# Kernel optimization log

Measured on AMD Instinct MI355X. Metric: run time of the kernel, lower is better.

The kernel has to match this reference:

```python
import jax, jax.numpy as jnp
import numpy as np

GROUPS = 32
EPS = 1e-6


def group_norm(x, scale, bias):
    B, C, H, W = x.shape
    xg = x.reshape(B, GROUPS, C // GROUPS, H, W)
    mean = xg.mean(axis=(2, 3, 4), keepdims=True)
    var = xg.var(axis=(2, 3, 4), keepdims=True)
    xg = (xg - mean) * jax.lax.rsqrt(var + EPS)
    x = xg.reshape(B, C, H, W)
    return x * scale[None, :, None, None] + bias[None, :, None, None]


def conv1x1(x, w, b):
    # x: [B,C,H,W], w: [O,C], b: [O]
    return jnp.einsum('bchw,oc->bohw', x, w) + b[None, :, None, None]


def setup_inputs() -> dict:
    key = jax.random.key(0)
    ks = jax.random.split(key, 6)
    B, C, H, W = 8, 256, 64, 64
    s = 1.0 / np.sqrt(C)
    return {
        'x': jax.random.normal(ks[0], (B, C, H, W), dtype=jnp.float32),
        'gn_scale': jnp.ones((C,), dtype=jnp.float32),
        'gn_bias': jnp.zeros((C,), dtype=jnp.float32),
        'wq': jax.random.normal(ks[1], (C, C), dtype=jnp.float32) * s,
        'bq': jnp.zeros((C,), dtype=jnp.float32),
        'wk': jax.random.normal(ks[2], (C, C), dtype=jnp.float32) * s,
        'bk': jnp.zeros((C,), dtype=jnp.float32),
        'wv': jax.random.normal(ks[3], (C, C), dtype=jnp.float32) * s,
        'bv': jnp.zeros((C,), dtype=jnp.float32),
        'wo': jax.random.normal(ks[4], (C, C), dtype=jnp.float32) * s,
        'bo': jnp.zeros((C,), dtype=jnp.float32),
    }


def reference(x, gn_scale, gn_bias, wq, bq, wk, bk, wv, bv, wo, bo):
    skip = x
    h = group_norm(x, gn_scale, gn_bias)
    B, C, H, W = h.shape
    N = H * W
    q = conv1x1(h, wq, bq).reshape(B, C, N)  # [B,C,N]
    k = conv1x1(h, wk, bk).reshape(B, C, N)
    v = conv1x1(h, wv, bv).reshape(B, C, N)
    # scores[b,i,j] = sum_c q[b,c,i] k[b,c,j] / sqrt(C)
    scores = jnp.einsum('bci,bcj->bij', q, k) / jnp.sqrt(jnp.float32(C))
    a = jax.nn.softmax(scores, axis=2)  # softmax over keys j
    # z[b,c,i] = sum_j v[b,c,j] a[b,i,j]
    z = jnp.einsum('bcj,bij->bci', v, a).reshape(B, C, H, W)
    z = conv1x1(z, wo, bo)
    return skip + z
```

## Files before the change

kernel.cpp:

```cpp
#include <hip/hip_runtime.h>
#include <math.h>

typedef __bf16 bf16;
typedef __bf16 bf16x8 __attribute__((ext_vector_type(8)));
typedef __bf16 bf16x4 __attribute__((ext_vector_type(4)));
typedef float  f32x4  __attribute__((ext_vector_type(4)));
typedef float  f32x16 __attribute__((ext_vector_type(16)));
typedef unsigned int u32;
typedef unsigned char u8;
typedef u32 u32x2 __attribute__((ext_vector_type(2)));
typedef u32 u32x4 __attribute__((ext_vector_type(4)));
typedef int  i32x8 __attribute__((ext_vector_type(8)));

#define MFMA(a, b, c)   __builtin_amdgcn_mfma_f32_16x16x32_bf16((a), (b), (c), 0, 0, 0)
#define MFMAS(a, b, c)                                                           \
  __builtin_amdgcn_mfma_scale_f32_32x32x64_f8f6f4((a), (b), (c), 0, 0,           \
                                                  0, 0x7f7f7f7f, 0, 0x7f7f7f7f)

#define GLOAD_LDS16(g, l)                                                        \
  __builtin_amdgcn_global_load_lds(                                              \
      (const __attribute__((address_space(1))) void*)(g),                        \
      (__attribute__((address_space(3))) void*)(l), 16, 0, 0)

static constexpr int B_ = 8, C_ = 256, N_ = 4096;
static constexpr float QSCALE = 0.09016844005556021f;
static constexpr float PBIAS  = 2.0f;


static constexpr size_t HT_OFF = 0;
static constexpr size_t QT_OFF = 16777216;
static constexpr size_t KT_OFF = 25165824;
static constexpr size_t V_OFF  = 33554432;
static constexpr size_t WQ_OFF = 41943040;
static constexpr size_t WK_OFF = WQ_OFF + 131072;
static constexpr size_t WV_OFF = WK_OFF + 131072;
static constexpr size_t WO_OFF = WV_OFF + 131072;
static constexpr size_t LS_OFF = WO_OFF + 131072;
static constexpr size_t ZN2_OFF = LS_OFF + 524288;
static constexpr size_t PART_ELEMS = (size_t)B_ * C_ * N_;

__global__ __launch_bounds__(512) void gn_kernel(
    const float* __restrict__ x, const float* __restrict__ gsc, const float* __restrict__ gbi,
    bf16* __restrict__ hT,
    const float* __restrict__ wq, const float* __restrict__ wk,
    const float* __restrict__ wv, const float* __restrict__ wo,
    bf16* __restrict__ oq, bf16* __restrict__ ok, bf16* __restrict__ ov, bf16* __restrict__ oo) {
  int b = blockIdx.x >> 5, g = blockIdx.x & 31, c0 = g * 8;
  int t = threadIdx.x;
  if (t < 256) {
    int i = blockIdx.x * 256 + t;
    oq[i] = (bf16)wq[i];
    ok[i] = (bf16)wk[i];
    ov[i] = (bf16)wv[i];
    oo[i] = (bf16)wo[i];
  }
  const float* base = x + ((size_t)(b * C_ + c0)) * N_;
  __shared__ bf16 xl[32768];
  float s = 0.f, ss = 0.f;
  const f32x4* b4 = (const f32x4*)base;
#pragma unroll
  for (int p = 0; p < 16; p++) {
    int u = t + p * 512;
    f32x4 v = b4[u];
    s  += v[0] + v[1] + v[2] + v[3];
    ss += v[0] * v[0] + v[1] * v[1] + v[2] * v[2] + v[3] * v[3];
    bf16x4 xv;
#pragma unroll
    for (int e = 0; e < 4; e++) xv[e] = (bf16)v[e];
    *(bf16x4*)(xl + u * 4) = xv;
  }
#pragma unroll
  for (int off = 1; off < 64; off <<= 1) {
    s  += __shfl_xor(s, off);
    ss += __shfl_xor(ss, off);
  }
  __shared__ float red[16];
  if ((t & 63) == 0) { red[(t >> 6) * 2] = s; red[(t >> 6) * 2 + 1] = ss; }
  __syncthreads();
  s = 0.f; ss = 0.f;
#pragma unroll
  for (int r = 0; r < 8; r++) { s += red[r * 2]; ss += red[r * 2 + 1]; }
  float mean = s * (1.f / 32768.f);
  float var  = ss * (1.f / 32768.f) - mean * mean;
  float rstd = rsqrtf(var + 1e-6f);
  float aa[8], bb[8];
#pragma unroll
  for (int cc = 0; cc < 8; cc++) {
    aa[cc] = rstd * gsc[c0 + cc];
    bb[cc] = gbi[c0 + cc] - mean * aa[cc];
  }
#pragma unroll
  for (int ii = 0; ii < 8; ii++) {
    int i = t + ii * 512;
    bf16x8 o;
#pragma unroll
    for (int cc = 0; cc < 8; cc++) o[cc] = (bf16)((float)xl[cc * 4096 + i] * aa[cc] + bb[cc]);
    *(bf16x8*)(hT + ((size_t)(b * N_ + i)) * C_ + c0) = o;
  }
}

__global__ __launch_bounds__(256, 4) void qkv_kernel(
    const bf16* __restrict__ hT,
    const bf16* __restrict__ wqb, const bf16* __restrict__ wkb, const bf16* __restrict__ wvb,
    const float* __restrict__ bq, const float* __restrict__ bk, const float* __restrict__ bv,
    u8* __restrict__ qT8, u8* __restrict__ kT8, u8* __restrict__ v8) {
  int b = blockIdx.x >> 6, i0 = (blockIdx.x & 63) << 6;
  int t = threadIdx.x, w = t >> 6, lane = t & 63, quad = lane >> 4, l15 = lane & 15;
  __shared__ bf16 hl[64 * 264];
  __shared__ __align__(16) u8 ep[16384];
#pragma unroll
  for (int p = 0; p < 8; p++) {
    int u = t + p * 256, r = u >> 5, c16 = u & 31;
    *(bf16x8*)(hl + r * 264 + c16 * 8) =
        *(const bf16x8*)(hT + ((size_t)(b * N_ + i0 + r)) * C_ + c16 * 8);
  }
  __syncthreads();
  int cw0 = w * 64;

  {
    f32x4 acc[4][4];
#pragma unroll
    for (int a = 0; a < 4; a++)
#pragma unroll
      for (int bb2 = 0; bb2 < 4; bb2++) acc[a][bb2] = (f32x4){0.f, 0.f, 0.f, 0.f};
#pragma unroll 2
    for (int kc = 0; kc < 8; kc++) {
      bf16x8 hb[4];
#pragma unroll
      for (int it = 0; it < 4; it++)
        hb[it] = *(const bf16x8*)(hl + (it * 16 + l15) * 264 + kc * 32 + quad * 8);
#pragma unroll
      for (int ct = 0; ct < 4; ct++) {
        bf16x8 wf = *(const bf16x8*)(wqb + ((size_t)(cw0 + ct * 16 + l15)) * C_ + kc * 32 + quad * 8);
#pragma unroll
        for (int it = 0; it < 4; it++) acc[ct][it] = MFMA(wf, hb[it], acc[ct][it]);
      }
    }
#pragma unroll
    for (int ct = 0; ct < 4; ct++)
#pragma unroll
      for (int it = 0; it < 4; it++) {
        int c4 = cw0 + ct * 16 + quad * 4;
        int il = it * 16 + l15;
        f32x4 b4v = *(const f32x4*)(bq + c4);
        float qv[4];
#pragma unroll
        for (int r = 0; r < 4; r++) qv[r] = (acc[ct][it][r] + b4v[r]) * (QSCALE * 4.0f);
        u32 qd = (u32)__builtin_amdgcn_cvt_pk_fp8_f32(qv[0], qv[1], 0, false);
        qd = (u32)__builtin_amdgcn_cvt_pk_fp8_f32(qv[2], qv[3], (int)qd, true);
        *(u32*)(ep + il * 256 + ((((c4 >> 4) ^ (il & 15)) << 4) | (c4 & 12))) = qd;
      }
    __syncthreads();
#pragma unroll
    for (int p = 0; p < 4; p++) {
      int u = p * 256 + t, il = u >> 4, ch = u & 15;
      *(u32x4*)(qT8 + ((size_t)(b * N_ + i0 + il)) * C_ + ch * 16) =
          *(const u32x4*)(ep + il * 256 + (((ch ^ (il & 15)) << 4)));
    }
    __syncthreads();
  }

  {
    f32x4 acc[4][4];
#pragma unroll
    for (int a = 0; a < 4; a++)
#pragma unroll
      for (int bb2 = 0; bb2 < 4; bb2++) acc[a][bb2] = (f32x4){0.f, 0.f, 0.f, 0.f};
#pragma unroll 2
    for (int kc = 0; kc < 8; kc++) {
      bf16x8 hb[4];
#pragma unroll
      for (int it = 0; it < 4; it++)
        hb[it] = *(const bf16x8*)(hl + (it * 16 + l15) * 264 + kc * 32 + quad * 8);
#pragma unroll
      for (int ct = 0; ct < 4; ct++) {
        bf16x8 wf = *(const bf16x8*)(wkb + ((size_t)(cw0 + ct * 16 + l15)) * C_ + kc * 32 + quad * 8);
#pragma unroll
        for (int it = 0; it < 4; it++) acc[ct][it] = MFMA(wf, hb[it], acc[ct][it]);
      }
    }
#pragma unroll
    for (int ct = 0; ct < 4; ct++)
#pragma unroll
      for (int it = 0; it < 4; it++) {
        int c4 = cw0 + ct * 16 + quad * 4;
        int il = it * 16 + l15;
        f32x4 b4v = *(const f32x4*)(bk + c4);
        float kv[4];
#pragma unroll
        for (int r = 0; r < 4; r++) kv[r] = (acc[ct][it][r] + b4v[r]) * 0.25f;
        u32 kd = (u32)__builtin_amdgcn_cvt_pk_fp8_f32(kv[0], kv[1], 0, false);
        kd = (u32)__builtin_amdgcn_cvt_pk_fp8_f32(kv[2], kv[3], (int)kd, true);
        *(u32*)(ep + il * 256 + ((((c4 >> 4) ^ (il & 15)) << 4) | (c4 & 12))) = kd;
      }
    __syncthreads();
#pragma unroll
    for (int p = 0; p < 4; p++) {
      int u = p * 256 + t, il = u >> 4, ch = u & 15;
      *(u32x4*)(kT8 + ((size_t)(b * N_ + i0 + il)) * C_ + ch * 16) =
          *(const u32x4*)(ep + il * 256 + (((ch ^ (il & 15)) << 4)));
    }
  }

  {
    f32x4 acc[4][4];
#pragma unroll
    for (int a = 0; a < 4; a++)
#pragma unroll
      for (int bb2 = 0; bb2 < 4; bb2++) acc[a][bb2] = (f32x4){0.f, 0.f, 0.f, 0.f};
#pragma unroll 2
    for (int kc = 0; kc < 8; kc++) {
      bf16x8 hb[4];
#pragma unroll
      for (int it = 0; it < 4; it++)
        hb[it] = *(const bf16x8*)(hl + (it * 16 + l15) * 264 + kc * 32 + quad * 8);
#pragma unroll
      for (int ct = 0; ct < 4; ct++) {
        bf16x8 wf = *(const bf16x8*)(wvb + ((size_t)(cw0 + ct * 16 + l15)) * C_ + kc * 32 + quad * 8);
#pragma unroll
        for (int it = 0; it < 4; it++) acc[it][ct] = MFMA(hb[it], wf, acc[it][ct]);
      }
    }
    __syncthreads();
#pragma unroll
    for (int it = 0; it < 4; it++)
#pragma unroll
      for (int ct = 0; ct < 4; ct++) {
        int cl = cw0 + ct * 16 + l15;
        float bvc = bv[cl];
        float vv4[4];
#pragma unroll
        for (int r = 0; r < 4; r++) vv4[r] = acc[it][ct][r] + bvc;
        u32 vd = (u32)__builtin_amdgcn_cvt_pk_fp8_f32(vv4[0], vv4[1], 0, false);
        vd = (u32)__builtin_amdgcn_cvt_pk_fp8_f32(vv4[2], vv4[3], (int)vd, true);
        *(u32*)(ep + cl * 64 + ((((it ^ (cl & 3)) << 4)) | (quad * 4))) = vd;
      }
    __syncthreads();
#pragma unroll
    for (int p = 0; p < 4; p++) {
      int u = p * 256 + t, cl = u >> 2, io = u & 3;
      *(u32x4*)(v8 + ((size_t)(b * C_ + cl)) * N_ + i0 + io * 16) =
          *(const u32x4*)(ep + cl * 64 + (((io ^ (cl & 3)) << 4)));
    }
  }
}

__global__ __launch_bounds__(256, 2) void attn_kernel(
    const u8* __restrict__ qT8, const u8* __restrict__ kT8, const u8* __restrict__ v8,
    bf16* __restrict__ zn0, bf16* __restrict__ znR, float* __restrict__ lsum) {
  constexpr int NJT = 32;
  int blk = blockIdx.x;
  int sp = blk >> 8;
  int b = blk & 7;
  int i0 = ((blk >> 3) & 31) << 7;
  int t = threadIdx.x, w = t >> 6, lane = t & 63;
  int r31 = lane & 31, h = lane >> 5;
  __shared__ __align__(16) u8 lds8[4 * 16384];

  int iw = i0 + w * 32;
  const u8* qrow = qT8 + ((size_t)(b * N_ + iw + r31)) * C_ + h * 32;
  i32x8 qB[4];
#pragma unroll
  for (int m = 0; m < 4; m++) qB[m] = *(const i32x8*)(qrow + m * 64);

  f32x16 of[8];
#pragma unroll
  for (int ct = 0; ct < 8; ct++)
#pragma unroll
    for (int e = 0; e < 16; e++) of[ct][e] = 0.f;
  float lacc = 0.f;

  int ks = r31 & 7;
  int kr_off = lane >> 4;
  int kc_pos = lane & 15;
  int vr_off = lane >> 2;
  int vc_pos = lane & 3;
  int spBase = sp * 2048;

  auto stageK = [&](int jts, u8* kb) {
    int j0s = spBase + jts * 64;
#pragma unroll
    for (int p = 0; p < 4; p++) {
      int idx = w * 4 + p;
      int r = idx * 4 + kr_off;
      int chunk = kc_pos ^ (r & 7);
      GLOAD_LDS16(kT8 + ((size_t)(b * N_ + j0s + r)) * C_ + chunk * 16, kb + idx * 1024);
    }
  };
  auto stageV = [&](int jts, u8* vb) {
    int j0s = spBase + jts * 64;
#pragma unroll
    for (int p = 0; p < 4; p++) {
      int idx = w * 4 + p;
      int c = idx * 16 + vr_off;
      int chunk = vc_pos ^ ((c >> 1) & 3);
      GLOAD_LDS16(v8 + ((size_t)(b * C_ + c)) * N_ + j0s + chunk * 16, vb + idx * 1024);
    }
  };

  stageK(0, lds8);
  stageV(0, lds8 + 32768);

  if (__popc(blk) & 1) __builtin_amdgcn_s_sleep(48);

  i32x8 pPrev;

  for (int jt = 0; jt < NJT; jt++) {
    stageK(jt < NJT - 1 ? jt + 1 : jt, lds8 + (((jt + 1) & 1) << 14));
    asm volatile("s_waitcnt vmcnt(8)" ::: "memory");
    __builtin_amdgcn_s_barrier();
    const u8* kTl = lds8 + ((jt & 1) << 14);
    const u8* vbp = lds8 + 32768 + (((jt + 1) & 1) << 14);

    f32x16 st0;
#pragma unroll
    for (int e = 0; e < 16; e++) st0[e] = -PBIAS;
    {
      const u8* krow = kTl + r31 * 256;
      __builtin_amdgcn_s_setprio(1);
#pragma unroll
      for (int m = 0; m < 4; m++) {
        int cd = m * 4 + h * 2;
        union { i32x8 v; u32x4 h4[2]; } kf;
        kf.h4[0] = *(const u32x4*)(krow + ((cd ^ ks) * 16));
        kf.h4[1] = *(const u32x4*)(krow + (((cd + 1) ^ ks) * 16));
        st0 = MFMAS(kf.v, qB[m], st0);
      }
    }
    if (jt) {
#pragma unroll
      for (int ct = 0; ct < 8; ct++) {
        int c = ct * 32 + r31;
        int vs = (c >> 1) & 3;
        const u8* vrow = vbp + c * 64;
        union { i32x8 v; u32x4 h4[2]; } vB;
        vB.h4[0] = *(const u32x4*)(vrow + (((2 * h) ^ vs) * 16));
        vB.h4[1] = *(const u32x4*)(vrow + (((2 * h + 1) ^ vs) * 16));
        of[ct] = MFMAS(pPrev, vB.v, of[ct]);
      }
    }
    __builtin_amdgcn_s_setprio(0);
    u32 PG0[4], PG1[4];
#pragma unroll
    for (int b4 = 0; b4 < 4; b4++) {
      float p0 = __builtin_amdgcn_exp2f(st0[b4 * 4 + 0]);
      float p1 = __builtin_amdgcn_exp2f(st0[b4 * 4 + 1]);
      float p2 = __builtin_amdgcn_exp2f(st0[b4 * 4 + 2]);
      float p3 = __builtin_amdgcn_exp2f(st0[b4 * 4 + 3]);
      lacc += (p0 + p1) + (p2 + p3);
      u32 d = (u32)__builtin_amdgcn_cvt_pk_fp8_f32(p0, p1, 0, false);
      d = (u32)__builtin_amdgcn_cvt_pk_fp8_f32(p2, p3, (int)d, true);
      PG0[b4] = d;
    }
    f32x16 st1;
#pragma unroll
    for (int e = 0; e < 16; e++) st1[e] = -PBIAS;
    {
      const u8* krow = kTl + (32 + r31) * 256;
      __builtin_amdgcn_s_setprio(1);
#pragma unroll
      for (int m = 0; m < 4; m++) {
        int cd = m * 4 + h * 2;
        union { i32x8 v; u32x4 h4[2]; } kf;
        kf.h4[0] = *(const u32x4*)(krow + ((cd ^ ks) * 16));
        kf.h4[1] = *(const u32x4*)(krow + (((cd + 1) ^ ks) * 16));
        st1 = MFMAS(kf.v, qB[m], st1);
      }
      __builtin_amdgcn_s_setprio(0);
    }
#pragma unroll
    for (int b4 = 0; b4 < 4; b4++) {
      float p0 = __builtin_amdgcn_exp2f(st1[b4 * 4 + 0]);
      float p1 = __builtin_amdgcn_exp2f(st1[b4 * 4 + 1]);
      float p2 = __builtin_amdgcn_exp2f(st1[b4 * 4 + 2]);
      float p3 = __builtin_amdgcn_exp2f(st1[b4 * 4 + 3]);
      lacc += (p0 + p1) + (p2 + p3);
      u32 d = (u32)__builtin_amdgcn_cvt_pk_fp8_f32(p0, p1, 0, false);
      d = (u32)__builtin_amdgcn_cvt_pk_fp8_f32(p2, p3, (int)d, true);
      PG1[b4] = d;
    }
#pragma unroll
    for (int b4 = 0; b4 < 4; b4++) {
      u32x2 rr = __builtin_amdgcn_permlane32_swap(PG0[b4], PG1[b4], false, false);
      pPrev[2 * b4]     = (int)rr[0];
      pPrev[2 * b4 + 1] = (int)rr[1];
    }

    __builtin_amdgcn_s_barrier();
    if (jt < NJT - 1) stageV(jt + 1, lds8 + 32768 + (((jt + 1) & 1) << 14));
  }

  asm volatile("s_waitcnt vmcnt(0)" ::: "memory");
  __builtin_amdgcn_s_barrier();
  {
    const u8* vbp = lds8 + 32768 + (((NJT - 1) & 1) << 14);
#pragma unroll
    for (int ct = 0; ct < 8; ct++) {
      int c = ct * 32 + r31;
      int vs = (c >> 1) & 3;
      const u8* vrow = vbp + c * 64;
      union { i32x8 v; u32x4 h4[2]; } vB;
      vB.h4[0] = *(const u32x4*)(vrow + (((2 * h) ^ vs) * 16));
      vB.h4[1] = *(const u32x4*)(vrow + (((2 * h + 1) ^ vs) * 16));
      of[ct] = MFMAS(pPrev, vB.v, of[ct]);
    }
  }

  lacc += __shfl_xor(lacc, 32);
  if (h == 0)
    lsum[((size_t)(sp * 8 + b)) * N_ + iw + r31] = lacc;
  bf16* zn = (sp == 0) ? zn0 : znR;
#pragma unroll
  for (int ct = 0; ct < 8; ct++) {
    int c = ct * 32 + r31;
#pragma unroll
    for (int g = 0; g < 4; g++) {
      bf16x4 zv;
#pragma unroll
      for (int e = 0; e < 4; e++) zv[e] = (bf16)of[ct][g * 4 + e];
      int i4 = iw + 8 * g + 4 * h;
      *(bf16x4*)(zn + ((size_t)(b * C_ + c)) * N_ + i4) = zv;
    }
  }
}

__global__ __launch_bounds__(256) void combine_kernel(
    const bf16* __restrict__ zn0, const bf16* __restrict__ znR,
    const float* __restrict__ lsum,
    const bf16* __restrict__ wob, const float* __restrict__ bo,
    const float* __restrict__ x, float* __restrict__ out) {
  int b = blockIdx.x >> 6, i0 = (blockIdx.x & 63) << 6;
  int t = threadIdx.x, w = t >> 6, lane = t & 63, quad = lane >> 4, l15 = lane & 15;
  __shared__ bf16 zl[64 * 266];
  __shared__ float linv[64];

  if (t < 64) {
    size_t ii = (size_t)b * N_ + i0 + t;
    linv[t] = 1.f / (lsum[ii] + lsum[ii + (size_t)8 * N_]);
  }
  __syncthreads();

#pragma unroll
  for (int p = 0; p < 16; p++) {
    int u = t + p * 256, c = u >> 4, ii = (u & 15) * 4;
    size_t base = ((size_t)(b * C_ + c)) * N_ + i0 + ii;
    bf16x4 z0 = *(const bf16x4*)(zn0 + base);
    bf16x4 z1 = *(const bf16x4*)(znR + base);
#pragma unroll
    for (int e = 0; e < 4; e++)
      zl[(ii + e) * 266 + c] = (bf16)(((float)z0[e] + (float)z1[e]) * linv[ii + e]);
  }
  __syncthreads();

  f32x4 oa[4][4];
#pragma unroll
  for (int a = 0; a < 4; a++)
#pragma unroll
    for (int bb2 = 0; bb2 < 4; bb2++) oa[a][bb2] = (f32x4){0.f, 0.f, 0.f, 0.f};
  for (int kc = 0; kc < 8; kc++) {
    bf16x8 za[4];
#pragma unroll
    for (int it = 0; it < 4; it++)
      za[it] = *(const bf16x8*)(zl + (it * 16 + l15) * 266 + kc * 32 + quad * 8);
#pragma unroll
    for (int ctl = 0; ctl < 4; ctl++) {
      bf16x8 wf = *(const bf16x8*)(wob + ((size_t)(w * 64 + ctl * 16 + l15)) * C_ + kc * 32 + quad * 8);
#pragma unroll
      for (int it = 0; it < 4; it++) oa[ctl][it] = MFMA(za[it], wf, oa[ctl][it]);
    }
  }
#pragma unroll
  for (int ctl = 0; ctl < 4; ctl++)
#pragma unroll
    for (int it = 0; it < 4; it++) {
      int c = w * 64 + ctl * 16 + l15;
      size_t base = ((size_t)(b * C_ + c)) * N_ + i0 + it * 16 + quad * 4;
      f32x4 xs = *(const f32x4*)(x + base);
      float boc = bo[c];
      f32x4 o4;
#pragma unroll
      for (int r = 0; r < 4; r++) o4[r] = oa[ctl][it][r] + boc + xs[r];
      *(f32x4*)(out + base) = o4;
    }
}

extern "C" void kernel_launch(void* const* d_in, const int* in_sizes, int n_in,
                              void* d_out, int out_size, void* d_ws, size_t ws_size,
                              hipStream_t stream) {
  const float* x   = (const float*)d_in[0];
  const float* gsc = (const float*)d_in[1];
  const float* gbi = (const float*)d_in[2];
  const float* wq  = (const float*)d_in[3];
  const float* bq  = (const float*)d_in[4];
  const float* wk  = (const float*)d_in[5];
  const float* bk  = (const float*)d_in[6];
  const float* wv  = (const float*)d_in[7];
  const float* bv  = (const float*)d_in[8];
  const float* wo  = (const float*)d_in[9];
  const float* bo  = (const float*)d_in[10];

  char* ws = (char*)d_ws;
  bf16* hT   = (bf16*)(ws + HT_OFF);
  u8*   qT8  = (u8*)(ws + QT_OFF);
  u8*   kT8  = (u8*)(ws + KT_OFF);
  u8*   v8   = (u8*)(ws + V_OFF);
  bf16* wqb  = (bf16*)(ws + WQ_OFF);
  bf16* wkb  = (bf16*)(ws + WK_OFF);
  bf16* wvb  = (bf16*)(ws + WV_OFF);
  bf16* wob  = (bf16*)(ws + WO_OFF);
  float* lsum = (float*)(ws + LS_OFF);
  bf16* zn0  = (bf16*)(ws + HT_OFF);
  bf16* znR  = (bf16*)(ws + ZN2_OFF);

  gn_kernel<<<256, 512, 0, stream>>>(x, gsc, gbi, hT, wq, wk, wv, wo, wqb, wkb, wvb, wob);
  qkv_kernel<<<512, 256, 0, stream>>>(hT, wqb, wkb, wvb, bq, bk, bv, qT8, kT8, v8);
  attn_kernel<<<512, 256, 0, stream>>>(qT8, kT8, v8, zn0, znR, lsum);
  combine_kernel<<<512, 256, 0, stream>>>(zn0, znR, lsum, wob, bo, x, (float*)d_out);
}
```

Before: 239.2 us.

## Fuse four kernels into one cooperative persistent kernel with grid syncs

Replaces the four separate launches (group norm, QKV projection, attention, combine) with a single cooperative kernel of 512 blocks that separates the phases with grid.sync(). The aim is to remove per-launch overhead and the gaps between kernel boundaries. The group-norm phase is rewritten to run with 256 threads and a single pass that computes sum and sum of squares, instead of the old 512-thread version. The cost is that every phase now shares one LDS footprint and one register budget (launch bounds 256,2), grid syncs add their own cost, and the old launch path is kept as a fallback if the cooperative launch fails.

```diff
diff --git a/kernel.cpp b/kernel.cpp
--- a/kernel.cpp
+++ b/kernel.cpp
@@ -1,5 +1,8 @@
 #include <hip/hip_runtime.h>
+#include <hip/hip_cooperative_groups.h>
 #include <math.h>
+
+namespace cg = cooperative_groups;
 
 typedef __bf16 bf16;
 typedef __bf16 bf16x8 __attribute__((ext_vector_type(8)));
@@ -38,6 +41,456 @@
 static constexpr size_t LS_OFF = WO_OFF + 131072;
 static constexpr size_t ZN2_OFF = LS_OFF + 524288;
 static constexpr size_t PART_ELEMS = (size_t)B_ * C_ * N_;
+
+__global__ __launch_bounds__(256, 2) void mega_kernel(
+    const float* __restrict__ x, const float* __restrict__ gsc, const float* __restrict__ gbi,
+    const float* __restrict__ wq, const float* __restrict__ wk,
+    const float* __restrict__ wv, const float* __restrict__ wo,
+    const float* __restrict__ bq, const float* __restrict__ bk,
+    const float* __restrict__ bv, const float* __restrict__ bo,
+    char* __restrict__ ws, float* __restrict__ out) {
+  bf16* hT   = (bf16*)(ws + HT_OFF);
+  u8*   qT8  = (u8*)(ws + QT_OFF);
+  u8*   kT8  = (u8*)(ws + KT_OFF);
+  u8*   v8   = (u8*)(ws + V_OFF);
+  bf16* wqb  = (bf16*)(ws + WQ_OFF);
+  bf16* wkb  = (bf16*)(ws + WK_OFF);
+  bf16* wvb  = (bf16*)(ws + WV_OFF);
+  bf16* wob  = (bf16*)(ws + WO_OFF);
+  float* lsum = (float*)(ws + LS_OFF);
+  bf16* zn0  = (bf16*)(ws + HT_OFF);
+  bf16* znR  = (bf16*)(ws + ZN2_OFF);
+
+  cg::grid_group grid = cg::this_grid();
+  int blk = blockIdx.x, t = threadIdx.x;
+  __shared__ __align__(16) u8 smem[65536];
+
+  if (blk < 256) {
+    int b = blk >> 5, g = blk & 31, c0 = g * 8;
+    {
+      int i = blk * 256 + t;
+      wqb[i] = (bf16)wq[i];
+      wkb[i] = (bf16)wk[i];
+      wvb[i] = (bf16)wv[i];
+      wob[i] = (bf16)wo[i];
+    }
+    float* red = (float*)smem;
+    const float* xbase = x + ((size_t)(b * C_ + c0)) * N_;
+    const f32x4* b4 = (const f32x4*)xbase;
+    float s = 0.f, ss = 0.f;
+#pragma unroll 8
+    for (int p = 0; p < 32; p++) {
+      f32x4 v = b4[t + p * 256];
+      s  += v[0] + v[1] + v[2] + v[3];
+      ss += v[0] * v[0] + v[1] * v[1] + v[2] * v[2] + v[3] * v[3];
+    }
+#pragma unroll
+    for (int off = 1; off < 64; off <<= 1) {
+      s  += __shfl_xor(s, off);
+      ss += __shfl_xor(ss, off);
+    }
+    if ((t & 63) == 0) { red[(t >> 6) * 2] = s; red[(t >> 6) * 2 + 1] = ss; }
+    __syncthreads();
+    s = 0.f; ss = 0.f;
+#pragma unroll
+    for (int r = 0; r < 4; r++) { s += red[r * 2]; ss += red[r * 2 + 1]; }
+    float mean = s * (1.f / 32768.f);
+    float var  = ss * (1.f / 32768.f) - mean * mean;
+    float rstd = rsqrtf(var + 1e-6f);
+    float aa[8], bb[8];
+#pragma unroll
+    for (int cc = 0; cc < 8; cc++) {
+      aa[cc] = rstd * gsc[c0 + cc];
+      bb[cc] = gbi[c0 + cc] - mean * aa[cc];
+    }
+#pragma unroll 4
+    for (int ii = 0; ii < 16; ii++) {
+      int i = t + ii * 256;
+      bf16x8 o;
+#pragma unroll
+      for (int cc = 0; cc < 8; cc++)
+        o[cc] = (bf16)(xbase[(size_t)cc * N_ + i] * aa[cc] + bb[cc]);
+      *(bf16x8*)(hT + ((size_t)(b * N_ + i)) * C_ + c0) = o;
+    }
+  }
+  grid.sync();
+
+  {
+    int b = blk >> 6, i0 = (blk & 63) << 6;
+    int w = t >> 6, lane = t & 63, quad = lane >> 4, l15 = lane & 15;
+    bf16* hl = (bf16*)smem;
+    u8* ep = smem + 33792;
+#pragma unroll
+    for (int p = 0; p < 8; p++) {
+      int u = t + p * 256, r = u >> 5, c16 = u & 31;
+      *(bf16x8*)(hl + r * 264 + c16 * 8) =
+          *(const bf16x8*)(hT + ((size_t)(b * N_ + i0 + r)) * C_ + c16 * 8);
+    }
+    __syncthreads();
+    int cw0 = w * 64;
+
+    {
+      f32x4 acc[4][4];
+#pragma unroll
+      for (int a = 0; a < 4; a++)
+#pragma unroll
+        for (int b2 = 0; b2 < 4; b2++) acc[a][b2] = (f32x4){0.f, 0.f, 0.f, 0.f};
+#pragma unroll 2
+      for (int kc = 0; kc < 8; kc++) {
+        bf16x8 hb[4];
+#pragma unroll
+        for (int it = 0; it < 4; it++)
+          hb[it] = *(const bf16x8*)(hl + (it * 16 + l15) * 264 + kc * 32 + quad * 8);
+#pragma unroll
+        for (int ct = 0; ct < 4; ct++) {
+          bf16x8 wf = *(const bf16x8*)(wqb + ((size_t)(cw0 + ct * 16 + l15)) * C_ + kc * 32 + quad * 8);
+#pragma unroll
+          for (int it = 0; it < 4; it++) acc[ct][it] = MFMA(wf, hb[it], acc[ct][it]);
+        }
+      }
+#pragma unroll
+      for (int ct = 0; ct < 4; ct++)
+#pragma unroll
+        for (int it = 0; it < 4; it++) {
+          int c4 = cw0 + ct * 16 + quad * 4;
+          int il = it * 16 + l15;
+          f32x4 b4v = *(const f32x4*)(bq + c4);
+          float qv[4];
+#pragma unroll
+          for (int r = 0; r < 4; r++) qv[r] = (acc[ct][it][r] + b4v[r]) * (QSCALE * 4.0f);
+          u32 qd = (u32)__builtin_amdgcn_cvt_pk_fp8_f32(qv[0], qv[1], 0, false);
+          qd = (u32)__builtin_amdgcn_cvt_pk_fp8_f32(qv[2], qv[3], (int)qd, true);
+          *(u32*)(ep + il * 256 + ((((c4 >> 4) ^ (il & 15)) << 4) | (c4 & 12))) = qd;
+        }
+      __syncthreads();
+#pragma unroll
+      for (int p = 0; p < 4; p++) {
+        int u = p * 256 + t, il = u >> 4, ch = u & 15;
+        *(u32x4*)(qT8 + ((size_t)(b * N_ + i0 + il)) * C_ + ch * 16) =
+            *(const u32x4*)(ep + il * 256 + (((ch ^ (il & 15)) << 4)));
+      }
+      __syncthreads();
+    }
+
+    {
+      f32x4 acc[4][4];
+#pragma unroll
+      for (int a = 0; a < 4; a++)
+#pragma unroll
+        for (int b2 = 0; b2 < 4; b2++) acc[a][b2] = (f32x4){0.f, 0.f, 0.f, 0.f};
+#pragma unroll 2
+      for (int kc = 0; kc < 8; kc++) {
+        bf16x8 hb[4];
+#pragma unroll
+        for (int it = 0; it < 4; it++)
+          hb[it] = *(const bf16x8*)(hl + (it * 16 + l15) * 264 + kc * 32 + quad * 8);
+#pragma unroll
+        for (int ct = 0; ct < 4; ct++) {
+          bf16x8 wf = *(const bf16x8*)(wkb + ((size_t)(cw0 + ct * 16 + l15)) * C_ + kc * 32 + quad * 8);
+#pragma unroll
+          for (int it = 0; it < 4; it++) acc[ct][it] = MFMA(wf, hb[it], acc[ct][it]);
+        }
+      }
+#pragma unroll
+      for (int ct = 0; ct < 4; ct++)
+#pragma unroll
+        for (int it = 0; it < 4; it++) {
+          int c4 = cw0 + ct * 16 + quad * 4;
+          int il = it * 16 + l15;
+          f32x4 b4v = *(const f32x4*)(bk + c4);
+          float kv[4];
+#pragma unroll
+          for (int r = 0; r < 4; r++) kv[r] = (acc[ct][it][r] + b4v[r]) * 0.25f;
+          u32 kd = (u32)__builtin_amdgcn_cvt_pk_fp8_f32(kv[0], kv[1], 0, false);
+          kd = (u32)__builtin_amdgcn_cvt_pk_fp8_f32(kv[2], kv[3], (int)kd, true);
+          *(u32*)(ep + il * 256 + ((((c4 >> 4) ^ (il & 15)) << 4) | (c4 & 12))) = kd;
+        }
+      __syncthreads();
+#pragma unroll
+      for (int p = 0; p < 4; p++) {
+        int u = p * 256 + t, il = u >> 4, ch = u & 15;
+        *(u32x4*)(kT8 + ((size_t)(b * N_ + i0 + il)) * C_ + ch * 16) =
+            *(const u32x4*)(ep + il * 256 + (((ch ^ (il & 15)) << 4)));
+      }
+    }
+
+    {
+      f32x4 acc[4][4];
+#pragma unroll
+      for (int a = 0; a < 4; a++)
+#pragma unroll
+        for (int b2 = 0; b2 < 4; b2++) acc[a][b2] = (f32x4){0.f, 0.f, 0.f, 0.f};
+#pragma unroll 2
+      for (int kc = 0; kc < 8; kc++) {
+        bf16x8 hb[4];
+#pragma unroll
+        for (int it = 0; it < 4; it++)
+          hb[it] = *(const bf16x8*)(hl + (it * 16 + l15) * 264 + kc * 32 + quad * 8);
+#pragma unroll
+        for (int ct = 0; ct < 4; ct++) {
+          bf16x8 wf = *(const bf16x8*)(wvb + ((size_t)(cw0 + ct * 16 + l15)) * C_ + kc * 32 + quad * 8);
+#pragma unroll
+          for (int it = 0; it < 4; it++) acc[it][ct] = MFMA(hb[it], wf, acc[it][ct]);
+        }
+      }
+      __syncthreads();
+#pragma unroll
+      for (int it = 0; it < 4; it++)
+#pragma unroll
+        for (int ct = 0; ct < 4; ct++) {
+          int cl = cw0 + ct * 16 + l15;
+          float bvc = bv[cl];
+          float vv4[4];
+#pragma unroll
+          for (int r = 0; r < 4; r++) vv4[r] = acc[it][ct][r] + bvc;
+          u32 vd = (u32)__builtin_amdgcn_cvt_pk_fp8_f32(vv4[0], vv4[1], 0, false);
+          vd = (u32)__builtin_amdgcn_cvt_pk_fp8_f32(vv4[2], vv4[3], (int)vd, true);
+          *(u32*)(ep + cl * 64 + ((((it ^ (cl & 3)) << 4)) | (quad * 4))) = vd;
+        }
+      __syncthreads();
+#pragma unroll
+      for (int p = 0; p < 4; p++) {
+        int u = p * 256 + t, cl = u >> 2, io = u & 3;
+        *(u32x4*)(v8 + ((size_t)(b * C_ + cl)) * N_ + i0 + io * 16) =
+            *(const u32x4*)(ep + cl * 64 + (((io ^ (cl & 3)) << 4)));
+      }
+    }
+  }
+  grid.sync();
+
+  {
+    constexpr int NJT = 32;
+    int sp = blk >> 8;
+    int b = blk & 7;
+    int i0 = ((blk >> 3) & 31) << 7;
+    int w = t >> 6, lane = t & 63;
+    int r31 = lane & 31, h = lane >> 5;
+    u8* lds8 = smem;
+
+    int iw = i0 + w * 32;
+    const u8* qrow = qT8 + ((size_t)(b * N_ + iw + r31)) * C_ + h * 32;
+    i32x8 qB[4];
+#pragma unroll
+    for (int m = 0; m < 4; m++) qB[m] = *(const i32x8*)(qrow + m * 64);
+
+    f32x16 of[8];
+#pragma unroll
+    for (int ct = 0; ct < 8; ct++)
+#pragma unroll
+      for (int e = 0; e < 16; e++) of[ct][e] = 0.f;
+    float lacc = 0.f;
+
+    int ks = r31 & 7;
+    int kr_off = lane >> 4;
+    int kc_pos = lane & 15;
+    int vr_off = lane >> 2;
+    int vc_pos = lane & 3;
+    int spBase = sp * 2048;
+
+    auto stageK = [&](int jts, u8* kb) {
+      int j0s = spBase + jts * 64;
+#pragma unroll
+      for (int p = 0; p < 4; p++) {
+        int idx = w * 4 + p;
+        int r = idx * 4 + kr_off;
+        int chunk = kc_pos ^ (r & 7);
+        GLOAD_LDS16(kT8 + ((size_t)(b * N_ + j0s + r)) * C_ + chunk * 16, kb + idx * 1024);
+      }
+    };
+    auto stageV = [&](int jts, u8* vb) {
+      int j0s = spBase + jts * 64;
+#pragma unroll
+      for (int p = 0; p < 4; p++) {
+        int idx = w * 4 + p;
+        int c = idx * 16 + vr_off;
+        int chunk = vc_pos ^ ((c >> 1) & 3);
+        GLOAD_LDS16(v8 + ((size_t)(b * C_ + c)) * N_ + j0s + chunk * 16, vb + idx * 1024);
+      }
+    };
+
+    stageK(0, lds8);
+    stageV(0, lds8 + 32768);
+    if (__popc(blk) & 1) __builtin_amdgcn_s_sleep(48);
+
+    i32x8 pPrev;
+
+    for (int jt = 0; jt < NJT; jt++) {
+      stageK(jt < NJT - 1 ? jt + 1 : jt, lds8 + (((jt + 1) & 1) << 14));
+      asm volatile("s_waitcnt vmcnt(8)" ::: "memory");
+      __builtin_amdgcn_s_barrier();
+      const u8* kTl = lds8 + ((jt & 1) << 14);
+      const u8* vbp = lds8 + 32768 + (((jt + 1) & 1) << 14);
+
+      f32x16 st0;
+#pragma unroll
+      for (int e = 0; e < 16; e++) st0[e] = -PBIAS;
+      {
+        const u8* krow = kTl + r31 * 256;
+        __builtin_amdgcn_s_setprio(1);
+#pragma unroll
+        for (int m = 0; m < 4; m++) {
+          int cd = m * 4 + h * 2;
+          union { i32x8 v; u32x4 h4[2]; } kf;
+          kf.h4[0] = *(const u32x4*)(krow + ((cd ^ ks) * 16));
+          kf.h4[1] = *(const u32x4*)(krow + (((cd + 1) ^ ks) * 16));
+          st0 = MFMAS(kf.v, qB[m], st0);
+        }
+      }
+      if (jt) {
+#pragma unroll
+        for (int ct = 0; ct < 8; ct++) {
+          int c = ct * 32 + r31;
+          int vs = (c >> 1) & 3;
+          const u8* vrow = vbp + c * 64;
+          union { i32x8 v; u32x4 h4[2]; } vB;
+          vB.h4[0] = *(const u32x4*)(vrow + (((2 * h) ^ vs) * 16));
+          vB.h4[1] = *(const u32x4*)(vrow + (((2 * h + 1) ^ vs) * 16));
+          of[ct] = MFMAS(pPrev, vB.v, of[ct]);
+        }
+      }
+      __builtin_amdgcn_s_setprio(0);
+      u32 PG0[4], PG1[4];
+#pragma unroll
+      for (int b4 = 0; b4 < 4; b4++) {
+        float p0 = __builtin_amdgcn_exp2f(st0[b4 * 4 + 0]);
+        float p1 = __builtin_amdgcn_exp2f(st0[b4 * 4 + 1]);
+        float p2 = __builtin_amdgcn_exp2f(st0[b4 * 4 + 2]);
+        float p3 = __builtin_amdgcn_exp2f(st0[b4 * 4 + 3]);
+        lacc += (p0 + p1) + (p2 + p3);
+        u32 d = (u32)__builtin_amdgcn_cvt_pk_fp8_f32(p0, p1, 0, false);
+        d = (u32)__builtin_amdgcn_cvt_pk_fp8_f32(p2, p3, (int)d, true);
+        PG0[b4] = d;
+      }
+      f32x16 st1;
+#pragma unroll
+      for (int e = 0; e < 16; e++) st1[e] = -PBIAS;
+      {
+        const u8* krow = kTl + (32 + r31) * 256;
+        __builtin_amdgcn_s_setprio(1);
+#pragma unroll
+        for (int m = 0; m < 4; m++) {
+          int cd = m * 4 + h * 2;
+          union { i32x8 v; u32x4 h4[2]; } kf;
+          kf.h4[0] = *(const u32x4*)(krow + ((cd ^ ks) * 16));
+          kf.h4[1] = *(const u32x4*)(krow + (((cd + 1) ^ ks) * 16));
+          st1 = MFMAS(kf.v, qB[m], st1);
+        }
+        __builtin_amdgcn_s_setprio(0);
+      }
+#pragma unroll
+      for (int b4 = 0; b4 < 4; b4++) {
+        float p0 = __builtin_amdgcn_exp2f(st1[b4 * 4 + 0]);
+        float p1 = __builtin_amdgcn_exp2f(st1[b4 * 4 + 1]);
+        float p2 = __builtin_amdgcn_exp2f(st1[b4 * 4 + 2]);
+        float p3 = __builtin_amdgcn_exp2f(st1[b4 * 4 + 3]);
+        lacc += (p0 + p1) + (p2 + p3);
+        u32 d = (u32)__builtin_amdgcn_cvt_pk_fp8_f32(p0, p1, 0, false);
+        d = (u32)__builtin_amdgcn_cvt_pk_fp8_f32(p2, p3, (int)d, true);
+        PG1[b4] = d;
+      }
+#pragma unroll
+      for (int b4 = 0; b4 < 4; b4++) {
+        u32x2 rr = __builtin_amdgcn_permlane32_swap(PG0[b4], PG1[b4], false, false);
+        pPrev[2 * b4]     = (int)rr[0];
+        pPrev[2 * b4 + 1] = (int)rr[1];
+      }
+
+      __builtin_amdgcn_s_barrier();
+      if (jt < NJT - 1) stageV(jt + 1, lds8 + 32768 + (((jt + 1) & 1) << 14));
+    }
+
+    asm volatile("s_waitcnt vmcnt(0)" ::: "memory");
+    __builtin_amdgcn_s_barrier();
+    {
+      const u8* vbp = lds8 + 32768 + (((NJT - 1) & 1) << 14);
+#pragma unroll
+      for (int ct = 0; ct < 8; ct++) {
+        int c = ct * 32 + r31;
+        int vs = (c >> 1) & 3;
+        const u8* vrow = vbp + c * 64;
+        union { i32x8 v; u32x4 h4[2]; } vB;
+        vB.h4[0] = *(const u32x4*)(vrow + (((2 * h) ^ vs) * 16));
+        vB.h4[1] = *(const u32x4*)(vrow + (((2 * h + 1) ^ vs) * 16));
+        of[ct] = MFMAS(pPrev, vB.v, of[ct]);
+      }
+    }
+
+    lacc += __shfl_xor(lacc, 32);
+    if (h == 0)
+      lsum[((size_t)(sp * 8 + b)) * N_ + iw + r31] = lacc;
+    bf16* zn = (sp == 0) ? zn0 : znR;
+#pragma unroll
+    for (int ct = 0; ct < 8; ct++) {
+      int c = ct * 32 + r31;
+#pragma unroll
+      for (int g = 0; g < 4; g++) {
+        bf16x4 zv;
+#pragma unroll
+        for (int e = 0; e < 4; e++) zv[e] = (bf16)of[ct][g * 4 + e];
+        int i4 = iw + 8 * g + 4 * h;
+        *(bf16x4*)(zn + ((size_t)(b * C_ + c)) * N_ + i4) = zv;
+      }
+    }
+  }
+  grid.sync();
+
+  {
+    int b = blk >> 6, i0 = (blk & 63) << 6;
+    int w = t >> 6, lane = t & 63, quad = lane >> 4, l15 = lane & 15;
+    bf16* zl = (bf16*)smem;
+    float* linv = (float*)(smem + 34048);
+
+    if (t < 64) {
+      size_t ii = (size_t)b * N_ + i0 + t;
+      linv[t] = 1.f / (lsum[ii] + lsum[ii + (size_t)8 * N_]);
+    }
+    __syncthreads();
+
+#pragma unroll
+    for (int p = 0; p < 16; p++) {
+      int u = t + p * 256, c = u >> 4, ii = (u & 15) * 4;
+      size_t base = ((size_t)(b * C_ + c)) * N_ + i0 + ii;
+      bf16x4 z0 = *(const bf16x4*)(zn0 + base);
+      bf16x4 z1 = *(const bf16x4*)(znR + base);
+#pragma unroll
+      for (int e = 0; e < 4; e++)
+        zl[(ii + e) * 266 + c] = (bf16)(((float)z0[e] + (float)z1[e]) * linv[ii + e]);
+    }
+    __syncthreads();
+
+    f32x4 oa[4][4];
+#pragma unroll
+    for (int a = 0; a < 4; a++)
+#pragma unroll
+      for (int b2 = 0; b2 < 4; b2++) oa[a][b2] = (f32x4){0.f, 0.f, 0.f, 0.f};
+#pragma unroll 2
+    for (int kc = 0; kc < 8; kc++) {
+      bf16x8 za[4];
+#pragma unroll
+      for (int it = 0; it < 4; it++)
+        za[it] = *(const bf16x8*)(zl + (it * 16 + l15) * 266 + kc * 32 + quad * 8);
+#pragma unroll
+      for (int ctl = 0; ctl < 4; ctl++) {
+        bf16x8 wf = *(const bf16x8*)(wob + ((size_t)(w * 64 + ctl * 16 + l15)) * C_ + kc * 32 + quad * 8);
+#pragma unroll
+        for (int it = 0; it < 4; it++) oa[ctl][it] = MFMA(za[it], wf, oa[ctl][it]);
+      }
+    }
+#pragma unroll
+    for (int ctl = 0; ctl < 4; ctl++)
+#pragma unroll
+      for (int it = 0; it < 4; it++) {
+        int c = w * 64 + ctl * 16 + l15;
+        size_t base = ((size_t)(b * C_ + c)) * N_ + i0 + it * 16 + quad * 4;
+        f32x4 xs = *(const f32x4*)(x + base);
+        float boc = bo[c];
+        f32x4 o4;
+#pragma unroll
+        for (int r = 0; r < 4; r++) o4[r] = oa[ctl][it][r] + boc + xs[r];
+        *(f32x4*)(out + base) = o4;
+      }
+  }
+}
 
 __global__ __launch_bounds__(512) void gn_kernel(
     const float* __restrict__ x, const float* __restrict__ gsc, const float* __restrict__ gbi,
@@ -116,13 +569,12 @@
   }
   __syncthreads();
   int cw0 = w * 64;
-
   {
     f32x4 acc[4][4];
 #pragma unroll
     for (int a = 0; a < 4; a++)
 #pragma unroll
-      for (int bb2 = 0; bb2 < 4; bb2++) acc[a][bb2] = (f32x4){0.f, 0.f, 0.f, 0.f};
+      for (int b2 = 0; b2 < 4; b2++) acc[a][b2] = (f32x4){0.f, 0.f, 0.f, 0.f};
 #pragma unroll 2
     for (int kc = 0; kc < 8; kc++) {
       bf16x8 hb[4];
@@ -159,13 +611,12 @@
     }
     __syncthreads();
   }
-
   {
     f32x4 acc[4][4];
 #pragma unroll
     for (int a = 0; a < 4; a++)
 #pragma unroll
-      for (int bb2 = 0; bb2 < 4; bb2++) acc[a][bb2] = (f32x4){0.f, 0.f, 0.f, 0.f};
+      for (int b2 = 0; b2 < 4; b2++) acc[a][b2] = (f32x4){0.f, 0.f, 0.f, 0.f};
 #pragma unroll 2
     for (int kc = 0; kc < 8; kc++) {
       bf16x8 hb[4];
@@ -201,13 +652,12 @@
           *(const u32x4*)(ep + il * 256 + (((ch ^ (il & 15)) << 4)));
     }
   }
-
   {
     f32x4 acc[4][4];
 #pragma unroll
     for (int a = 0; a < 4; a++)
 #pragma unroll
-      for (int bb2 = 0; bb2 < 4; bb2++) acc[a][bb2] = (f32x4){0.f, 0.f, 0.f, 0.f};
+      for (int b2 = 0; b2 < 4; b2++) acc[a][b2] = (f32x4){0.f, 0.f, 0.f, 0.f};
 #pragma unroll 2
     for (int kc = 0; kc < 8; kc++) {
       bf16x8 hb[4];
@@ -300,7 +750,6 @@
 
   stageK(0, lds8);
   stageV(0, lds8 + 32768);
-
   if (__popc(blk) & 1) __builtin_amdgcn_s_sleep(48);
 
   i32x8 pPrev;
@@ -456,7 +905,8 @@
 #pragma unroll
   for (int a = 0; a < 4; a++)
 #pragma unroll
-    for (int bb2 = 0; bb2 < 4; bb2++) oa[a][bb2] = (f32x4){0.f, 0.f, 0.f, 0.f};
+    for (int b2 = 0; b2 < 4; b2++) oa[a][b2] = (f32x4){0.f, 0.f, 0.f, 0.f};
+#pragma unroll 2
   for (int kc = 0; kc < 8; kc++) {
     bf16x8 za[4];
 #pragma unroll
@@ -498,22 +948,32 @@
   const float* bv  = (const float*)d_in[8];
   const float* wo  = (const float*)d_in[9];
   const float* bo  = (const float*)d_in[10];
-
   char* ws = (char*)d_ws;
-  bf16* hT   = (bf16*)(ws + HT_OFF);
-  u8*   qT8  = (u8*)(ws + QT_OFF);
-  u8*   kT8  = (u8*)(ws + KT_OFF);
-  u8*   v8   = (u8*)(ws + V_OFF);
-  bf16* wqb  = (bf16*)(ws + WQ_OFF);
-  bf16* wkb  = (bf16*)(ws + WK_OFF);
-  bf16* wvb  = (bf16*)(ws + WV_OFF);
-  bf16* wob  = (bf16*)(ws + WO_OFF);
-  float* lsum = (float*)(ws + LS_OFF);
-  bf16* zn0  = (bf16*)(ws + HT_OFF);
-  bf16* znR  = (bf16*)(ws + ZN2_OFF);
-
-  gn_kernel<<<256, 512, 0, stream>>>(x, gsc, gbi, hT, wq, wk, wv, wo, wqb, wkb, wvb, wob);
-  qkv_kernel<<<512, 256, 0, stream>>>(hT, wqb, wkb, wvb, bq, bk, bv, qT8, kT8, v8);
-  attn_kernel<<<512, 256, 0, stream>>>(qT8, kT8, v8, zn0, znR, lsum);
-  combine_kernel<<<512, 256, 0, stream>>>(zn0, znR, lsum, wob, bo, x, (float*)d_out);
+  float* outp = (float*)d_out;
+
+  void* args[] = {
+    (void*)&x, (void*)&gsc, (void*)&gbi,
+    (void*)&wq, (void*)&wk, (void*)&wv, (void*)&wo,
+    (void*)&bq, (void*)&bk, (void*)&bv, (void*)&bo,
+    (void*)&ws, (void*)&outp};
+  hipError_t e = hipLaunchCooperativeKernel((void*)mega_kernel, dim3(512), dim3(256),
+                                            args, 0, stream);
+  if (e != hipSuccess) {
+    (void)hipGetLastError();
+    bf16* hT   = (bf16*)(ws + HT_OFF);
+    u8*   qT8  = (u8*)(ws + QT_OFF);
+    u8*   kT8  = (u8*)(ws + KT_OFF);
+    u8*   v8   = (u8*)(ws + V_OFF);
+    bf16* wqb  = (bf16*)(ws + WQ_OFF);
+    bf16* wkb  = (bf16*)(ws + WK_OFF);
+    bf16* wvb  = (bf16*)(ws + WV_OFF);
+    bf16* wob  = (bf16*)(ws + WO_OFF);
+    float* lsum = (float*)(ws + LS_OFF);
+    bf16* zn0  = (bf16*)(ws + HT_OFF);
+    bf16* znR  = (bf16*)(ws + ZN2_OFF);
+    gn_kernel<<<256, 512, 0, stream>>>(x, gsc, gbi, hT, wq, wk, wv, wo, wqb, wkb, wvb, wob);
+    qkv_kernel<<<512, 256, 0, stream>>>(hT, wqb, wkb, wvb, bq, bk, bv, qT8, kT8, v8);
+    attn_kernel<<<512, 256, 0, stream>>>(qT8, kT8, v8, zn0, znR, lsum);
+    combine_kernel<<<512, 256, 0, stream>>>(zn0, znR, lsum, wob, bo, x, (float*)d_out);
+  }
 }
```

Result: slower. 465.2 us (+94.4%).
